# Performance work log

Hardware: AMD Instinct MI355X
Metric: run time of the kernel (lower is better)

## Reference

```python
import jax, jax.numpy as jnp
import numpy as np

ROT_DIM = 32  # rotary sub-dimension hardcoded in the original module


def apply_rope(x, rope):
    # x: [B, T, H, hd], rope: [T, ROT_DIM//2, 2]
    T = x.shape[1]
    rc = rope[:T][:, None]            # [T, 1, 16, 2]
    cos, sin = rc[..., 0], rc[..., 1]  # [T, 1, 16]
    x_rot, x_pass = x[..., :ROT_DIM], x[..., ROT_DIM:]
    x1, x2 = x_rot[..., :ROT_DIM // 2], x_rot[..., ROT_DIM // 2:]
    return jnp.concatenate([x1 * cos - x2 * sin, x2 * cos + x1 * sin, x_pass], axis=-1)


def setup_inputs() -> dict:
    key = jax.random.key(0)
    ks = jax.random.split(key, 6)
    B, T, C, H = 4, 1024, 2048, 32
    hd = C // H
    x = jax.random.normal(ks[0], (B, T, C), dtype=jnp.float32)
    mask = jnp.tril(jnp.ones((T, T), dtype=bool))  # causal, True = attend
    index = jnp.arange(T, dtype=jnp.int64) if jax.config.jax_enable_x64 else jnp.arange(T, dtype=jnp.int32)
    # realistic rotary cos/sin cache
    inv_freq = 1.0 / (10000.0 ** (np.arange(0, ROT_DIM, 2, dtype=np.float32) / ROT_DIM))
    ang = np.arange(T, dtype=np.float32)[:, None] * inv_freq[None, :]  # [T, 16]
    rope = jnp.asarray(np.stack([np.cos(ang), np.sin(ang)], axis=-1))   # [T, 16, 2]
    s = 1.0 / np.sqrt(C)
    Wqkv_w = jax.random.normal(ks[1], (3 * C, C), dtype=jnp.float32) * s
    Wqkv_b = jax.random.normal(ks[2], (3 * C,), dtype=jnp.float32) * 0.01
    out_w = jax.random.normal(ks[3], (C, C), dtype=jnp.float32) * s
    out_b = jax.random.normal(ks[4], (C,), dtype=jnp.float32) * 0.01
    k_cache = jnp.zeros((B, H, T, hd), dtype=jnp.float32)
    v_cache = jnp.zeros((B, H, T, hd), dtype=jnp.float32)
    return {"x": x, "mask": mask, "index": index, "rope": rope,
            "Wqkv_w": Wqkv_w, "Wqkv_b": Wqkv_b, "out_w": out_w, "out_b": out_b,
            "k_cache": k_cache, "v_cache": v_cache}


def reference(x, mask, index, rope, Wqkv_w, Wqkv_b, out_w, out_b, k_cache, v_cache):
    B, T, C = x.shape
    H = 32
    hd = C // H
    qkv = x @ Wqkv_w.T + Wqkv_b                 # [B, T, 3C]
    q, k, v = jnp.split(qkv, 3, axis=-1)
    q = q.reshape(B, T, H, hd)
    k = k.reshape(B, T, H, hd)
    v = v.reshape(B, T, H, hd)
    q = apply_rope(q, rope)
    k = apply_rope(k, rope)
    q = q.transpose(0, 2, 1, 3)                 # [B, H, T, hd]
    k = k.transpose(0, 2, 1, 3)
    v = v.transpose(0, 2, 1, 3)
    # KV-cache scatter update; index = arange(T) covers the full cache, so the
    # subsequent slice [:, :, :index[-1]+1] is the whole cache (static shape).
    k_full = k_cache.at[:, :, index].set(k)
    v_full = v_cache.at[:, :, index].set(v)
    scores = jnp.einsum('bhqd,bhkd->bhqk', q, k_full) / jnp.sqrt(jnp.asarray(hd, x.dtype))
    scores = jnp.where(mask, scores, jnp.finfo(x.dtype).min)
    attn = jax.nn.softmax(scores, axis=-1)
    ctx = jnp.einsum('bhqk,bhkd->bhqd', attn, v_full)
    ctx = ctx.transpose(0, 2, 1, 3).reshape(B, T, C)
    return ctx @ out_w.T + out_b
```

## Files before the change

kernel.cpp:

```cpp
#include <hip/hip_runtime.h>

typedef unsigned short u16;
typedef unsigned int u32;
typedef __bf16 bf16x8 __attribute__((ext_vector_type(8)));
typedef float floatx4 __attribute__((ext_vector_type(4)));
typedef u16 u16x4 __attribute__((ext_vector_type(4)));
typedef u16 u16x8 __attribute__((ext_vector_type(8)));
typedef u32 u32x2 __attribute__((ext_vector_type(2)));

#define B_ 4
#define T_ 1024
#define C_ 2048
#define H_ 32
#define HD_ 64

__device__ __forceinline__ float b2f(u16 u) {
    u32 x = ((u32)u) << 16;
    return __builtin_bit_cast(float, x);
}
__device__ __forceinline__ u16 f2b(float f) {
    u32 i = __builtin_bit_cast(u32, f);
    u32 r = (i + 0x7FFFu + ((i >> 16) & 1u)) >> 16;
    return (u16)r;
}
__device__ __forceinline__ u32 pack2(float a, float b) {
    const u32 ua = __builtin_bit_cast(u32, a) + 0x8000u;
    const u32 ub = __builtin_bit_cast(u32, b) + 0x8000u;
    return __builtin_amdgcn_perm(ub, ua, 0x07060302u);
}

#define GLOAD16(gp, lp) __builtin_amdgcn_global_load_lds( \
    (const __attribute__((address_space(1))) void*)(gp),  \
    (__attribute__((address_space(3))) void*)(lp), 16, 0, 0)

__global__ __launch_bounds__(256) void convert_bf16(const float* __restrict__ src,
                                                    u16* __restrict__ dst, int n4) {
    const int stride = gridDim.x * 256;
    for (int i = blockIdx.x * 256 + threadIdx.x; i < n4; i += stride) {
        const floatx4 v = *(const floatx4*)(src + (size_t)i * 4);
        const u32x2 h = {pack2(v.x, v.y), pack2(v.z, v.w)};
        *(u32x2*)(dst + (size_t)i * 4) = h;
    }
}

template <int MODE>
__global__ __launch_bounds__(256) void gemm_bt(const u16* __restrict__ A,
                                               const u16* __restrict__ W,
                                               const float* __restrict__ bias,
                                               const float* __restrict__ rope,
                                               void* __restrict__ o0v,
                                               u16* __restrict__ o1,
                                               u16* __restrict__ o2) {
    const int Kdim = 2048;
    __shared__ __align__(16) u16 As[128 * 64];
    __shared__ __align__(16) u16 Bs[128 * 64];

    const int tid = threadIdx.x;
    const int w = tid >> 6, lane = tid & 63;
    const int wr = w >> 1, wc = w & 1;
    const int quad = lane >> 4, l15 = lane & 15;
    const int mBase = blockIdx.y * 128, nBase = blockIdx.x * 128;

    floatx4 acc[4][4] = {};

    const int lrow = lane >> 3;
    const int lcol = ((lane & 7) ^ lrow) * 8;
    const u16* Ap = A + (size_t)(mBase + lrow) * Kdim + lcol;
    const u16* Wp = W + (size_t)(nBase + lrow) * Kdim + lcol;

    const int xk = l15 & 7;

    for (int k0 = 0; k0 < Kdim; k0 += 64) {
#pragma unroll
        for (int i = 0; i < 4; i++) {
            const int c = i * 4 + w;
            GLOAD16(Ap + (size_t)c * 8 * Kdim + k0, &As[c * 512]);
            GLOAD16(Wp + (size_t)c * 8 * Kdim + k0, &Bs[c * 512]);
        }
        __syncthreads();
#pragma unroll
        for (int ks = 0; ks < 64; ks += 32) {
            bf16x8 af[4], bfr[4];
#pragma unroll
            for (int i = 0; i < 4; i++) {
                const int co = (((ks >> 3) + quad) ^ xk) * 8;
                af[i] = *(const bf16x8*)&As[(wr * 64 + i * 16 + l15) * 64 + co];
            }
#pragma unroll
            for (int j = 0; j < 4; j++) {
                const int co = (((ks >> 3) + quad) ^ xk) * 8;
                bfr[j] = *(const bf16x8*)&Bs[(wc * 64 + j * 16 + l15) * 64 + co];
            }
#pragma unroll
            for (int i = 0; i < 4; i++)
#pragma unroll
                for (int j = 0; j < 4; j++)
                    acc[i][j] = __builtin_amdgcn_mfma_f32_16x16x32_bf16(af[i], bfr[j], acc[i][j], 0, 0, 0);
        }
        __syncthreads();
    }

    const int nq = nBase + wc * 64;
    float bv[4];
#pragma unroll
    for (int j = 0; j < 4; j++) bv[j] = bias[nq + j * 16 + l15];

    if (MODE == 0) {
        const int region = nq >> 11;
        const int h = (nq & 2047) >> 6;
        const int d = l15;
        u16* dst = (region == 0) ? (u16*)o0v : ((region == 1) ? o1 : o2);
#pragma unroll
        for (int i = 0; i < 4; i++) {
#pragma unroll
            for (int r = 0; r < 4; r++) {
                const int m = mBase + wr * 64 + i * 16 + quad * 4 + r;
                const int b = m >> 10, t = m & 1023;
                float v0 = acc[i][0][r] + bv[0];
                float v1 = acc[i][1][r] + bv[1];
                float v2 = acc[i][2][r] + bv[2];
                float v3 = acc[i][3][r] + bv[3];
                const size_t base = ((size_t)(b * H_ + h) * T_ + t) * HD_;
                if (region < 2) {
                    const float cz = rope[t * 32 + d * 2];
                    const float sz = rope[t * 32 + d * 2 + 1];
                    const float n0 = v0 * cz - v1 * sz;
                    const float n1 = v1 * cz + v0 * sz;
                    dst[base + d] = f2b(n0);
                    dst[base + 16 + d] = f2b(n1);
                } else {
                    dst[base + d] = f2b(v0);
                    dst[base + 16 + d] = f2b(v1);
                }
                dst[base + 32 + d] = f2b(v2);
                dst[base + 48 + d] = f2b(v3);
            }
        }
    } else {
        float* outf = (float*)o0v;
#pragma unroll
        for (int i = 0; i < 4; i++)
#pragma unroll
            for (int r = 0; r < 4; r++) {
                const int m = mBase + wr * 64 + i * 16 + quad * 4 + r;
                const size_t o = (size_t)m * 2048 + nq;
#pragma unroll
                for (int j = 0; j < 4; j++)
                    outf[o + j * 16 + l15] = acc[i][j][r] + bv[j];
            }
    }
}

#define VT_STR 72

__global__ __launch_bounds__(256) void attn_mfma(const u16* __restrict__ qT,
                                                 const u16* __restrict__ kT,
                                                 const u16* __restrict__ vT,
                                                 u16* __restrict__ ctx) {
    __shared__ __align__(16) u16 Vt[64 * VT_STR];
    __shared__ __align__(16) u16 Pt[4 * 16 * VT_STR];

    const int tid = threadIdx.x;
    const int w = tid >> 6, lane = tid & 63;
    const int quad = lane >> 4, l15 = lane & 15;
    const int qt = 15 - (int)blockIdx.x;
    const int bh = blockIdx.y;
    const size_t headBase = (size_t)bh * (T_ * HD_);

    bf16x8 qf[2];
    {
        const u16* qrow = qT + headBase + ((size_t)qt * 64 + w * 16 + l15) * HD_ + quad * 8;
        qf[0] = __builtin_bit_cast(bf16x8, *(const u16x8*)(qrow));
        qf[1] = __builtin_bit_cast(bf16x8, *(const u16x8*)(qrow + 32));
    }

    u16* myPt = &Pt[w * 16 * VT_STR];
    const int vhd = tid & 63, vkb = tid >> 6;
    float m_i = -1e30f, l_i = 0.f;
    floatx4 oacc[4] = {};

    for (int kt = 0; kt <= qt; kt++) {
        const u16* kp = kT + headBase + (size_t)kt * 64 * HD_;
        const u16* vp = vT + headBase + (size_t)kt * 64 * HD_;

        u16 vreg[16];
#pragma unroll
        for (int c = 0; c < 16; c++)
            vreg[c] = vp[(vkb * 16 + c) * HD_ + vhd];

        floatx4 st[4] = {};
#pragma unroll
        for (int mi = 0; mi < 4; mi++) {
            const u16* krow = kp + (mi * 16 + l15) * HD_ + quad * 8;
            const bf16x8 kf0 = __builtin_bit_cast(bf16x8, *(const u16x8*)(krow));
            const bf16x8 kf1 = __builtin_bit_cast(bf16x8, *(const u16x8*)(krow + 32));
            st[mi] = __builtin_amdgcn_mfma_f32_16x16x32_bf16(kf0, qf[0], st[mi], 0, 0, 0);
            st[mi] = __builtin_amdgcn_mfma_f32_16x16x32_bf16(kf1, qf[1], st[mi], 0, 0, 0);
        }

        __syncthreads();
#pragma unroll
        for (int c4 = 0; c4 < 4; c4++) {
            const u16x4 vv = {vreg[c4 * 4], vreg[c4 * 4 + 1], vreg[c4 * 4 + 2], vreg[c4 * 4 + 3]};
            *(u16x4*)&Vt[vhd * VT_STR + vkb * 16 + c4 * 4] = vv;
        }
        __syncthreads();

        float pmax = -1e30f;
#pragma unroll
        for (int mi = 0; mi < 4; mi++)
#pragma unroll
            for (int r = 0; r < 4; r++) {
                float sv = st[mi][r] * 0.125f;
                if (kt == qt && (mi * 16 + quad * 4 + r) > (w * 16 + l15)) sv = -1e30f;
                st[mi][r] = sv;
                pmax = fmaxf(pmax, sv);
            }
        pmax = fmaxf(pmax, __shfl_xor(pmax, 16, 64));
        pmax = fmaxf(pmax, __shfl_xor(pmax, 32, 64));
        const float mnew = fmaxf(m_i, pmax);
        const float alpha = __expf(m_i - mnew);
        m_i = mnew;

        float psum = 0.f;
#pragma unroll
        for (int mi = 0; mi < 4; mi++) {
            u16x4 pk;
#pragma unroll
            for (int r = 0; r < 4; r++) {
                const float p = __expf(st[mi][r] - mnew);
                psum += p;
                pk[r] = f2b(p);
            }
            *(u16x4*)&myPt[l15 * VT_STR + mi * 16 + quad * 4] = pk;
        }
        psum += __shfl_xor(psum, 16, 64);
        psum += __shfl_xor(psum, 32, 64);
        l_i = l_i * alpha + psum;

#pragma unroll
        for (int mi = 0; mi < 4; mi++) oacc[mi] *= alpha;

        bf16x8 pf[2];
        pf[0] = __builtin_bit_cast(bf16x8, *(const u16x8*)&myPt[l15 * VT_STR + quad * 8]);
        pf[1] = __builtin_bit_cast(bf16x8, *(const u16x8*)&myPt[l15 * VT_STR + 32 + quad * 8]);
#pragma unroll
        for (int mi = 0; mi < 4; mi++) {
            const bf16x8 vf0 = __builtin_bit_cast(bf16x8, *(const u16x8*)&Vt[(mi * 16 + l15) * VT_STR + quad * 8]);
            const bf16x8 vf1 = __builtin_bit_cast(bf16x8, *(const u16x8*)&Vt[(mi * 16 + l15) * VT_STR + 32 + quad * 8]);
            oacc[mi] = __builtin_amdgcn_mfma_f32_16x16x32_bf16(vf0, pf[0], oacc[mi], 0, 0, 0);
            oacc[mi] = __builtin_amdgcn_mfma_f32_16x16x32_bf16(vf1, pf[1], oacc[mi], 0, 0, 0);
        }
    }

    const float inv = 1.0f / l_i;
    const int b = bh >> 5, h = bh & 31;
    const int t = qt * 64 + w * 16 + l15;
    u16* cp = ctx + ((size_t)(b * T_ + t)) * C_ + h * HD_;
#pragma unroll
    for (int mi = 0; mi < 4; mi++) {
        const u16x4 ov = {f2b(oacc[mi][0] * inv), f2b(oacc[mi][1] * inv),
                          f2b(oacc[mi][2] * inv), f2b(oacc[mi][3] * inv)};
        *(u16x4*)(cp + mi * 16 + quad * 4) = ov;
    }
}

extern "C" void kernel_launch(void* const* d_in, const int* in_sizes, int n_in,
                              void* d_out, int out_size, void* d_ws, size_t ws_size,
                              hipStream_t stream) {
    const float* x      = (const float*)d_in[0];
    const float* rope   = (const float*)d_in[3];
    const float* Wqkv_w = (const float*)d_in[4];
    const float* Wqkv_b = (const float*)d_in[5];
    const float* out_w  = (const float*)d_in[6];
    const float* out_b  = (const float*)d_in[7];
    float* out = (float*)d_out;

    const size_t headElems = (size_t)B_ * H_ * T_ * HD_;
    u16* xb    = (u16*)d_ws;
    u16* wqkvb = xb + headElems;
    u16* outwb = wqkvb + 12582912;
    u16* qTp   = outwb + 4194304;
    u16* kTp   = qTp + headElems;
    u16* vTp   = kTp + headElems;
    u16* ctx   = xb;

    convert_bf16<<<dim3(2048), 256, 0, stream>>>(x, xb, 2097152);
    convert_bf16<<<dim3(3072), 256, 0, stream>>>(Wqkv_w, wqkvb, 3145728);
    convert_bf16<<<dim3(1024), 256, 0, stream>>>(out_w, outwb, 1048576);

    gemm_bt<0><<<dim3(48, 32), 256, 0, stream>>>(xb, wqkvb, Wqkv_b, rope, qTp, kTp, vTp);
    attn_mfma<<<dim3(16, 128), 256, 0, stream>>>(qTp, kTp, vTp, ctx);
    gemm_bt<1><<<dim3(16, 32), 256, 0, stream>>>(ctx, outwb, out_b, rope, out, nullptr, nullptr);
}
```

Measured before the change: 476.4 us.

## Pair causal query tiles per block, double-buffer V tile, use exp2 softmax

Each attention block now processes two query tiles, qt and 15-qt, so every block does the same amount of causal work, and the grid is halved. The transposed V tile in shared memory is double-buffered, which removes one __syncthreads per key tile. Softmax now uses exp2 with the log2(e) factor folded into the scale, and probabilities are written with a packed bf16 conversion. The trade-off is fewer blocks in flight and more shared memory per block, which may reduce occupancy and latency hiding.

```diff
diff --git a/kernel.cpp b/kernel.cpp
--- a/kernel.cpp
+++ b/kernel.cpp
@@ -157,111 +157,119 @@
                                                  const u16* __restrict__ kT,
                                                  const u16* __restrict__ vT,
                                                  u16* __restrict__ ctx) {
-    __shared__ __align__(16) u16 Vt[64 * VT_STR];
+    __shared__ __align__(16) u16 Vt[2][64 * VT_STR];
     __shared__ __align__(16) u16 Pt[4 * 16 * VT_STR];
 
     const int tid = threadIdx.x;
     const int w = tid >> 6, lane = tid & 63;
     const int quad = lane >> 4, l15 = lane & 15;
-    const int qt = 15 - (int)blockIdx.x;
     const int bh = blockIdx.y;
     const size_t headBase = (size_t)bh * (T_ * HD_);
 
-    bf16x8 qf[2];
-    {
-        const u16* qrow = qT + headBase + ((size_t)qt * 64 + w * 16 + l15) * HD_ + quad * 8;
-        qf[0] = __builtin_bit_cast(bf16x8, *(const u16x8*)(qrow));
-        qf[1] = __builtin_bit_cast(bf16x8, *(const u16x8*)(qrow + 32));
-    }
-
     u16* myPt = &Pt[w * 16 * VT_STR];
     const int vhd = tid & 63, vkb = tid >> 6;
-    float m_i = -1e30f, l_i = 0.f;
-    floatx4 oacc[4] = {};
-
-    for (int kt = 0; kt <= qt; kt++) {
-        const u16* kp = kT + headBase + (size_t)kt * 64 * HD_;
-        const u16* vp = vT + headBase + (size_t)kt * 64 * HD_;
-
-        u16 vreg[16];
-#pragma unroll
-        for (int c = 0; c < 16; c++)
-            vreg[c] = vp[(vkb * 16 + c) * HD_ + vhd];
-
-        floatx4 st[4] = {};
+    const float SC = 0.18033688011112042f;
+
+    int gb = 0;
+#pragma unroll 1
+    for (int ti = 0; ti < 2; ti++) {
+        const int qt = ti ? (15 - (int)blockIdx.x) : (int)blockIdx.x;
+
+        bf16x8 qf[2];
+        {
+            const u16* qrow = qT + headBase + ((size_t)qt * 64 + w * 16 + l15) * HD_ + quad * 8;
+            qf[0] = __builtin_bit_cast(bf16x8, *(const u16x8*)(qrow));
+            qf[1] = __builtin_bit_cast(bf16x8, *(const u16x8*)(qrow + 32));
+        }
+
+        float m_i = -1e30f, l_i = 0.f;
+        floatx4 oacc[4] = {};
+
+        for (int kt = 0; kt <= qt; kt++) {
+            const u16* kp = kT + headBase + (size_t)kt * 64 * HD_;
+            const u16* vp = vT + headBase + (size_t)kt * 64 * HD_;
+
+            u16 vreg[16];
+#pragma unroll
+            for (int c = 0; c < 16; c++)
+                vreg[c] = vp[(vkb * 16 + c) * HD_ + vhd];
+
+            floatx4 st[4] = {};
+#pragma unroll
+            for (int mi = 0; mi < 4; mi++) {
+                const u16* krow = kp + (mi * 16 + l15) * HD_ + quad * 8;
+                const bf16x8 kf0 = __builtin_bit_cast(bf16x8, *(const u16x8*)(krow));
+                const bf16x8 kf1 = __builtin_bit_cast(bf16x8, *(const u16x8*)(krow + 32));
+                st[mi] = __builtin_amdgcn_mfma_f32_16x16x32_bf16(kf0, qf[0], st[mi], 0, 0, 0);
+                st[mi] = __builtin_amdgcn_mfma_f32_16x16x32_bf16(kf1, qf[1], st[mi], 0, 0, 0);
+            }
+
+            u16* vt = Vt[gb];
+#pragma unroll
+            for (int c4 = 0; c4 < 4; c4++) {
+                const u16x4 vv = {vreg[c4 * 4], vreg[c4 * 4 + 1], vreg[c4 * 4 + 2], vreg[c4 * 4 + 3]};
+                *(u16x4*)&vt[vhd * VT_STR + vkb * 16 + c4 * 4] = vv;
+            }
+            __syncthreads();
+
+            float pmax = -1e30f;
+#pragma unroll
+            for (int mi = 0; mi < 4; mi++)
+#pragma unroll
+                for (int r = 0; r < 4; r++) {
+                    float sv = st[mi][r] * SC;
+                    if (kt == qt && (mi * 16 + quad * 4 + r) > (w * 16 + l15)) sv = -1e30f;
+                    st[mi][r] = sv;
+                    pmax = fmaxf(pmax, sv);
+                }
+            pmax = fmaxf(pmax, __shfl_xor(pmax, 16, 64));
+            pmax = fmaxf(pmax, __shfl_xor(pmax, 32, 64));
+            const float mnew = fmaxf(m_i, pmax);
+            const float alpha = __builtin_amdgcn_exp2f(m_i - mnew);
+            m_i = mnew;
+
+            float psum = 0.f;
+#pragma unroll
+            for (int mi = 0; mi < 4; mi++) {
+                float p[4];
+#pragma unroll
+                for (int r = 0; r < 4; r++) {
+                    p[r] = __builtin_amdgcn_exp2f(st[mi][r] - mnew);
+                    psum += p[r];
+                }
+                const u32x2 pk2 = {pack2(p[0], p[1]), pack2(p[2], p[3])};
+                *(u32x2*)&myPt[l15 * VT_STR + mi * 16 + quad * 4] = pk2;
+            }
+            psum += __shfl_xor(psum, 16, 64);
+            psum += __shfl_xor(psum, 32, 64);
+            l_i = l_i * alpha + psum;
+
+#pragma unroll
+            for (int mi = 0; mi < 4; mi++) oacc[mi] *= alpha;
+
+            bf16x8 pf[2];
+            pf[0] = __builtin_bit_cast(bf16x8, *(const u16x8*)&myPt[l15 * VT_STR + quad * 8]);
+            pf[1] = __builtin_bit_cast(bf16x8, *(const u16x8*)&myPt[l15 * VT_STR + 32 + quad * 8]);
+#pragma unroll
+            for (int mi = 0; mi < 4; mi++) {
+                const bf16x8 vf0 = __builtin_bit_cast(bf16x8, *(const u16x8*)&vt[(mi * 16 + l15) * VT_STR + quad * 8]);
+                const bf16x8 vf1 = __builtin_bit_cast(bf16x8, *(const u16x8*)&vt[(mi * 16 + l15) * VT_STR + 32 + quad * 8]);
+                oacc[mi] = __builtin_amdgcn_mfma_f32_16x16x32_bf16(vf0, pf[0], oacc[mi], 0, 0, 0);
+                oacc[mi] = __builtin_amdgcn_mfma_f32_16x16x32_bf16(vf1, pf[1], oacc[mi], 0, 0, 0);
+            }
+            gb ^= 1;
+        }
+
+        const float inv = 1.0f / l_i;
+        const int b = bh >> 5, h = bh & 31;
+        const int t = qt * 64 + w * 16 + l15;
+        u16* cp = ctx + ((size_t)(b * T_ + t)) * C_ + h * HD_;
 #pragma unroll
         for (int mi = 0; mi < 4; mi++) {
-            const u16* krow = kp + (mi * 16 + l15) * HD_ + quad * 8;
-            const bf16x8 kf0 = __builtin_bit_cast(bf16x8, *(const u16x8*)(krow));
-            const bf16x8 kf1 = __builtin_bit_cast(bf16x8, *(const u16x8*)(krow + 32));
-            st[mi] = __builtin_amdgcn_mfma_f32_16x16x32_bf16(kf0, qf[0], st[mi], 0, 0, 0);
-            st[mi] = __builtin_amdgcn_mfma_f32_16x16x32_bf16(kf1, qf[1], st[mi], 0, 0, 0);
-        }
-
-        __syncthreads();
-#pragma unroll
-        for (int c4 = 0; c4 < 4; c4++) {
-            const u16x4 vv = {vreg[c4 * 4], vreg[c4 * 4 + 1], vreg[c4 * 4 + 2], vreg[c4 * 4 + 3]};
-            *(u16x4*)&Vt[vhd * VT_STR + vkb * 16 + c4 * 4] = vv;
-        }
-        __syncthreads();
-
-        float pmax = -1e30f;
-#pragma unroll
-        for (int mi = 0; mi < 4; mi++)
-#pragma unroll
-            for (int r = 0; r < 4; r++) {
-                float sv = st[mi][r] * 0.125f;
-                if (kt == qt && (mi * 16 + quad * 4 + r) > (w * 16 + l15)) sv = -1e30f;
-                st[mi][r] = sv;
-                pmax = fmaxf(pmax, sv);
-            }
-        pmax = fmaxf(pmax, __shfl_xor(pmax, 16, 64));
-        pmax = fmaxf(pmax, __shfl_xor(pmax, 32, 64));
-        const float mnew = fmaxf(m_i, pmax);
-        const float alpha = __expf(m_i - mnew);
-        m_i = mnew;
-
-        float psum = 0.f;
-#pragma unroll
-        for (int mi = 0; mi < 4; mi++) {
-            u16x4 pk;
-#pragma unroll
-            for (int r = 0; r < 4; r++) {
-                const float p = __expf(st[mi][r] - mnew);
-                psum += p;
-                pk[r] = f2b(p);
-            }
-            *(u16x4*)&myPt[l15 * VT_STR + mi * 16 + quad * 4] = pk;
-        }
-        psum += __shfl_xor(psum, 16, 64);
-        psum += __shfl_xor(psum, 32, 64);
-        l_i = l_i * alpha + psum;
-
-#pragma unroll
-        for (int mi = 0; mi < 4; mi++) oacc[mi] *= alpha;
-
-        bf16x8 pf[2];
-        pf[0] = __builtin_bit_cast(bf16x8, *(const u16x8*)&myPt[l15 * VT_STR + quad * 8]);
-        pf[1] = __builtin_bit_cast(bf16x8, *(const u16x8*)&myPt[l15 * VT_STR + 32 + quad * 8]);
-#pragma unroll
-        for (int mi = 0; mi < 4; mi++) {
-            const bf16x8 vf0 = __builtin_bit_cast(bf16x8, *(const u16x8*)&Vt[(mi * 16 + l15) * VT_STR + quad * 8]);
-            const bf16x8 vf1 = __builtin_bit_cast(bf16x8, *(const u16x8*)&Vt[(mi * 16 + l15) * VT_STR + 32 + quad * 8]);
-            oacc[mi] = __builtin_amdgcn_mfma_f32_16x16x32_bf16(vf0, pf[0], oacc[mi], 0, 0, 0);
-            oacc[mi] = __builtin_amdgcn_mfma_f32_16x16x32_bf16(vf1, pf[1], oacc[mi], 0, 0, 0);
-        }
-    }
-
-    const float inv = 1.0f / l_i;
-    const int b = bh >> 5, h = bh & 31;
-    const int t = qt * 64 + w * 16 + l15;
-    u16* cp = ctx + ((size_t)(b * T_ + t)) * C_ + h * HD_;
-#pragma unroll
-    for (int mi = 0; mi < 4; mi++) {
-        const u16x4 ov = {f2b(oacc[mi][0] * inv), f2b(oacc[mi][1] * inv),
-                          f2b(oacc[mi][2] * inv), f2b(oacc[mi][3] * inv)};
-        *(u16x4*)(cp + mi * 16 + quad * 4) = ov;
+            const u16x4 ov = {f2b(oacc[mi][0] * inv), f2b(oacc[mi][1] * inv),
+                              f2b(oacc[mi][2] * inv), f2b(oacc[mi][3] * inv)};
+            *(u16x4*)(cp + mi * 16 + quad * 4) = ov;
+        }
     }
 }
 
@@ -290,6 +298,6 @@
     convert_bf16<<<dim3(1024), 256, 0, stream>>>(out_w, outwb, 1048576);
 
     gemm_bt<0><<<dim3(48, 32), 256, 0, stream>>>(xb, wqkvb, Wqkv_b, rope, qTp, kTp, vTp);
-    attn_mfma<<<dim3(16, 128), 256, 0, stream>>>(qTp, kTp, vTp, ctx);
+    attn_mfma<<<dim3(8, 128), 256, 0, stream>>>(qTp, kTp, vTp, ctx);
     gemm_bt<1><<<dim3(16, 32), 256, 0, stream>>>(ctx, outwb, out_b, rope, out, nullptr, nullptr);
 }
```

New measurement: 433.6 us. 1.1x faster.
